# Optimization experiments

Hardware: AMD Instinct MI355X
Metric: run time of the kernel (lower is better)

The kernel has to match this reference:

```python
import jax, jax.numpy as jnp
import numpy as np

N = 100000
E = 1_600_000
DIN = 24
DH = 64
DOUT = 12
NEG_SLOPE = 0.01  # torch F.leaky_relu default


def setup_inputs() -> dict:
    key = jax.random.key(0)
    ks = jax.random.split(key, 18)
    inp = {}
    inp["feats"] = jax.random.normal(ks[0], (N, DIN), dtype=jnp.float32)
    inp["e_w"] = jax.random.uniform(ks[1], (E, 1), dtype=jnp.float32)
    inp["snorm_n"] = jnp.ones((N, 1), dtype=jnp.float32)
    inp["snorm_e"] = jnp.ones((E, 1), dtype=jnp.float32)
    inp["src"] = jax.random.randint(ks[2], (E,), 0, N, dtype=jnp.int32)
    inp["dst"] = jax.random.randint(ks[3], (E,), 0, N, dtype=jnp.int32)
    s = 0.05
    inp["emb_h_W"] = jax.random.normal(ks[4], (DH, DIN), dtype=jnp.float32) * s
    inp["emb_h_b"] = jnp.zeros((DH,), dtype=jnp.float32)
    inp["emb_e_W"] = jax.random.normal(ks[5], (DH, 1), dtype=jnp.float32) * s
    inp["emb_e_b"] = jnp.zeros((DH,), dtype=jnp.float32)
    inp["W_self1"] = jax.random.normal(ks[6], (DH, DH), dtype=jnp.float32) * s
    inp["W_func1"] = jax.random.normal(ks[7], (DH, DH), dtype=jnp.float32) * s
    inp["attn1"] = jax.random.normal(ks[8], (3 * DH,), dtype=jnp.float32) * s
    inp["W_self2"] = jax.random.normal(ks[9], (DH, DH), dtype=jnp.float32) * s
    inp["W_func2"] = jax.random.normal(ks[10], (DH, DH), dtype=jnp.float32) * s
    inp["attn2"] = jax.random.normal(ks[11], (3 * DH,), dtype=jnp.float32) * s
    inp["lin1_W"] = jax.random.normal(ks[12], (DOUT, DH), dtype=jnp.float32) * s
    inp["lin1_b"] = jnp.zeros((DOUT,), dtype=jnp.float32)
    return inp


def _gat_layer(h, w_edge, src, dst, W_self, W_func, attn):
    # h: [N, d], w_edge: [E, d] edge embedding, attn: [3d]
    h_s = h @ W_self.T                       # linear_self(h)
    z = h @ W_func.T                         # linear_func(h)
    d = z.shape[-1]
    a_src, a_dst, a_w = attn[:d], attn[d:2 * d], attn[2 * d:]
    # attention score: W_a . [z_src, z_dst, w]  (decomposed to avoid [E,3d] concat)
    s_node_src = z @ a_src                   # [N]
    s_node_dst = z @ a_dst                   # [N]
    e = s_node_src[src] + s_node_dst[dst] + w_edge @ a_w  # [E]
    e = jax.nn.leaky_relu(e, NEG_SLOPE)
    # segment softmax over incoming edges per destination node
    m = jax.ops.segment_max(e, dst, num_segments=h.shape[0])
    ex = jnp.exp(e - m[dst])
    denom = jax.ops.segment_sum(ex, dst, num_segments=h.shape[0])
    alpha = ex / denom[dst]                  # [E]
    msg = alpha[:, None] * z[src]            # [E, d]
    agg = jax.ops.segment_sum(msg, dst, num_segments=h.shape[0])  # [N, d]
    # DGL: nodes with no incoming edges keep their old 'h' (not h_s + agg)
    in_deg = jax.ops.segment_sum(jnp.ones_like(e), dst, num_segments=h.shape[0])
    h_mid = jnp.where((in_deg > 0)[:, None], h_s + agg, h)
    return h + jax.nn.relu(h_mid)            # relu then residual


def reference(feats, e_w, snorm_n, snorm_e, src, dst,
              emb_h_W, emb_h_b, emb_e_W, emb_e_b,
              W_self1, W_func1, attn1, W_self2, W_func2, attn2,
              lin1_W, lin1_b):
    feats = feats.reshape(feats.shape[0], -1)
    h = feats @ emb_h_W.T + emb_h_b          # [N, DH]
    e = e_w @ emb_e_W.T + emb_e_b            # [E, DH]
    h = _gat_layer(h, e, src, dst, W_self1, W_func1, attn1)
    h = _gat_layer(h, e, src, dst, W_self2, W_func2, attn2)
    y = h @ lin1_W.T + lin1_b                # [N, DOUT]
    return y
```

## Files before the change

### kernel.cpp

```cpp
#include <hip/hip_runtime.h>
#include <hip/hip_fp16.h>

#define N_NODES 100000
#define N_EDGES 1600000
#define DIN 24
#define DH 64
#define DOUT 12
#define NEG_SLOPE 0.01f
#define NG 32
#define EPG (N_EDGES / NG)
#define NS 7
#define SLICE_N 16384
#define NTOT (NG * N_NODES)
#define SCAN_BLK 4096
#define LDSW 72

#define NB_HIST (NS * NG)
#define NB_EMBED (((N_NODES * DH) + 8191) / 8192)
#define NB_SUMDEG ((N_NODES + 255) / 256)
#define NB_SCAN1N ((N_NODES + SCAN_BLK - 1) / SCAN_BLK)
#define NB_SCAT ((N_EDGES + 255) / 256)
#define NB_NODE ((N_NODES + 63) / 64)
#define NB_NODE_T ((NB_NODE + 1) / 2)
#define NB_AGG ((N_NODES + 7) / 8)

typedef _Float16 half8_t __attribute__((ext_vector_type(8)));
typedef float floatx4 __attribute__((ext_vector_type(4)));

__device__ __forceinline__ void dev_consts(const float* emb_e_W, const float* emb_e_b,
                                           const float* attn1, const float* attn2,
                                           float* consts) {
    int lane = threadIdx.x;
    if (lane >= 64) return;
    float w = emb_e_W[lane], b = emb_e_b[lane];
    float a1 = attn1[2 * DH + lane], a2 = attn2[2 * DH + lane];
    float c11 = w * a1, c01 = b * a1, c12 = w * a2, c02 = b * a2;
    for (int off = 32; off; off >>= 1) {
        c11 += __shfl_down(c11, off);
        c01 += __shfl_down(c01, off);
        c12 += __shfl_down(c12, off);
        c02 += __shfl_down(c02, off);
    }
    if (lane == 0) {
        consts[0] = c11; consts[1] = c01; consts[2] = c12; consts[3] = c02;
    }
}

__device__ __forceinline__ void dev_hist(int bid, const int* dst,
                                         unsigned char* deg, unsigned char* rank) {
    __shared__ unsigned cnt[SLICE_N / 4];
    int s = bid % NS, c = bid / NS;
    for (int i = threadIdx.x; i < SLICE_N / 4; i += 1024) cnt[i] = 0;
    __syncthreads();
    int nbase = s * SLICE_N;
    int start = c * EPG, end = start + EPG;
    for (int i = start + threadIdx.x; i < end; i += 1024) {
        int local = dst[i] - nbase;
        if ((unsigned)local < SLICE_N) {
            unsigned sh = (unsigned)(local & 3) * 8u;
            unsigned old = atomicAdd(&cnt[local >> 2], 1u << sh);
            rank[i] = (unsigned char)((old >> sh) & 255u);
        }
    }
    __syncthreads();
    int nmax = N_NODES - nbase;
    if (nmax > SLICE_N) nmax = SLICE_N;
    unsigned* dw = (unsigned*)(deg + (size_t)c * N_NODES + nbase);
    for (int l = threadIdx.x; l < (nmax >> 2); l += 1024) dw[l] = cnt[l];
}

__device__ __forceinline__ void dev_embed(int bid, const float* feats, const float* W,
                                          const float* b, float* h) {
    for (int r = 0; r < 8; ++r) {
        int idx = bid * 8192 + r * 1024 + threadIdx.x;
        if (idx >= N_NODES * DH) return;
        int n = idx >> 6, o = idx & 63;
        const float* f = feats + n * DIN;
        const float* w = W + o * DIN;
        float acc = b[o];
#pragma unroll
        for (int k = 0; k < DIN; ++k) acc += f[k] * w[k];
        h[idx] = acc;
    }
}

__device__ __forceinline__ void dev_scan1(int bid, const int* in, int* out,
                                          int* part, int n) {
    __shared__ int lds[256];
    int t = threadIdx.x;
    int base = bid * SCAN_BLK + t * 16;
    int v[16];
    int s = 0;
#pragma unroll
    for (int i = 0; i < 16; ++i) {
        int idx = base + i;
        v[i] = (idx < n) ? in[idx] : 0;
        s += v[i];
    }
    lds[t] = s;
    __syncthreads();
    for (int off = 1; off < 256; off <<= 1) {
        int y = (t >= off) ? lds[t - off] : 0;
        __syncthreads();
        lds[t] += y;
        __syncthreads();
    }
    int run = lds[t] - s;
#pragma unroll
    for (int i = 0; i < 16; ++i) {
        int idx = base + i;
        if (idx < n) out[idx] = run;
        run += v[i];
    }
    if (t == 255) part[bid] = lds[255];
}

__device__ __forceinline__ void dev_scan2(int* part, int nblk, int* row_offN) {
    __shared__ int lds2[256];
    int t = threadIdx.x;
    int v[4];
    int s = 0;
#pragma unroll
    for (int i = 0; i < 4; ++i) {
        int idx = t * 4 + i;
        v[i] = (idx < nblk) ? part[idx] : 0;
        s += v[i];
    }
    lds2[t] = s;
    __syncthreads();
    for (int off = 1; off < 256; off <<= 1) {
        int y = (t >= off) ? lds2[t - off] : 0;
        __syncthreads();
        lds2[t] += y;
        __syncthreads();
    }
    int run = lds2[t] - s;
#pragma unroll
    for (int i = 0; i < 4; ++i) {
        int idx = t * 4 + i;
        if (idx < nblk) part[idx] = run;
        run += v[i];
    }
    if (row_offN) {
        __syncthreads();
        if (t == 0) row_offN[N_NODES] = N_EDGES - part[N_NODES >> 12];
    }
}

__device__ __forceinline__ void dev_sumdeg(int bid, const unsigned char* degB,
                                           int* degN, unsigned char* chunkOff) {
    int n = bid * 256 + threadIdx.x;
    if (n >= N_NODES) return;
    int run = 0;
#pragma unroll
    for (int g = 0; g < NG; ++g) {
        size_t idx = (size_t)g * N_NODES + n;
        int v = (int)degB[idx];
        chunkOff[idx] = (unsigned char)run;
        run += v;
    }
    degN[n] = run;
}

__device__ __forceinline__ void dev_nodeM(int bid, int stride, const float* h,
                                          const float* Wself, const float* Wfunc,
                                          const float* attn,
                                          __half* zh, float* hs,
                                          float* s_src, float* s_dst) {
    __shared__ _Float16 lds[2 * 64 * LDSW];
    int tid = threadIdx.x;
    for (int idx = tid; idx < 2 * 64 * 64; idx += 256) {
        int mat = idx >> 12, rem = idx & 4095;
        int o = rem >> 6, k = rem & 63;
        float v = mat ? Wfunc[rem] : Wself[rem];
        lds[(mat * 64 + o) * LDSW + k] = (_Float16)v;
    }
    __syncthreads();

    int wave = tid >> 6, lane = tid & 63;
    int quad = lane >> 4, lm = lane & 15;
    float asv[4], adv[4];
#pragma unroll
    for (int t = 0; t < 4; ++t) {
        asv[t] = attn[t * 16 + lm];
        adv[t] = attn[DH + t * 16 + lm];
    }
    const _Float16* bS = lds;
    const _Float16* bF = lds + 64 * LDSW;

    for (int tb = bid; tb < NB_NODE; tb += stride) {
        int n0 = (tb * 4 + wave) * 16;
        if (n0 >= N_NODES) continue;

        half8_t afrag[2];
        {
            const float4* hrow = (const float4*)(h + (size_t)(n0 + lm) * DH);
#pragma unroll
            for (int ks = 0; ks < 2; ++ks) {
                float4 p0 = hrow[ks * 8 + quad * 2];
                float4 p1 = hrow[ks * 8 + quad * 2 + 1];
                half8_t a;
                a[0] = (_Float16)p0.x; a[1] = (_Float16)p0.y;
                a[2] = (_Float16)p0.z; a[3] = (_Float16)p0.w;
                a[4] = (_Float16)p1.x; a[5] = (_Float16)p1.y;
                a[6] = (_Float16)p1.z; a[7] = (_Float16)p1.w;
                afrag[ks] = a;
            }
        }

        floatx4 accS[4], accF[4];
#pragma unroll
        for (int t = 0; t < 4; ++t) { accS[t] = (floatx4)0.f; accF[t] = (floatx4)0.f; }

#pragma unroll
        for (int t = 0; t < 4; ++t) {
            int o = t * 16 + lm;
#pragma unroll
            for (int ks = 0; ks < 2; ++ks) {
                int hoff = o * LDSW + ks * 32 + quad * 8;
                half8_t b1 = *(const half8_t*)(bS + hoff);
                half8_t b2 = *(const half8_t*)(bF + hoff);
                accS[t] = __builtin_amdgcn_mfma_f32_16x16x32_f16(afrag[ks], b1, accS[t], 0, 0, 0);
                accF[t] = __builtin_amdgcn_mfma_f32_16x16x32_f16(afrag[ks], b2, accF[t], 0, 0, 0);
            }
        }

        float ps[4] = {0.f, 0.f, 0.f, 0.f}, pd[4] = {0.f, 0.f, 0.f, 0.f};
#pragma unroll
        for (int t = 0; t < 4; ++t) {
#pragma unroll
            for (int r = 0; r < 4; ++r) {
                int node = n0 + quad * 4 + r;
                float zv = accF[t][r];
                zh[(size_t)node * DH + t * 16 + lm] = __float2half(zv);
                hs[(size_t)node * DH + t * 16 + lm] = accS[t][r];
                ps[r] += zv * asv[t];
                pd[r] += zv * adv[t];
            }
        }
#pragma unroll
        for (int r = 0; r < 4; ++r) {
            float p1 = ps[r], p2 = pd[r];
            for (int off = 8; off; off >>= 1) {
                p1 += __shfl_xor(p1, off);
                p2 += __shfl_xor(p2, off);
            }
            if (lm == 0) {
                s_src[n0 + quad * 4 + r] = p1;
                s_dst[n0 + quad * 4 + r] = p2;
            }
        }
    }
}

__global__ void __launch_bounds__(1024, 2)
k_fuse1(const float* __restrict__ feats, const float* __restrict__ emb_h_W,
        const float* __restrict__ emb_h_b, float* __restrict__ h,
        const int* __restrict__ dst, unsigned char* __restrict__ deg,
        unsigned char* __restrict__ rank,
        const float* __restrict__ emb_e_W, const float* __restrict__ emb_e_b,
        const float* __restrict__ attn1, const float* __restrict__ attn2,
        float* __restrict__ consts) {
    int bid = blockIdx.x;
    if (bid == 0) { dev_consts(emb_e_W, emb_e_b, attn1, attn2, consts); return; }
    bid -= 1;
    if (bid < NB_HIST) { dev_hist(bid, dst, deg, rank); return; }
    dev_embed(bid - NB_HIST, feats, emb_h_W, emb_h_b, h);
}

__global__ void __launch_bounds__(256, 4)
k_fuse2(const unsigned char* __restrict__ degB, int* __restrict__ degN,
        unsigned char* __restrict__ chunkOff,
        const float* __restrict__ h, const float* __restrict__ Wself1,
        const float* __restrict__ Wfunc1, const float* __restrict__ attn1,
        __half* __restrict__ zh, float* __restrict__ hs,
        float* __restrict__ s_src, float* __restrict__ s_dst) {
    int bid = blockIdx.x;
    if (bid < NB_SUMDEG) { dev_sumdeg(bid, degB, degN, chunkOff); return; }
    dev_nodeM(bid - NB_SUMDEG, NB_NODE_T, h, Wself1, Wfunc1, attn1,
              zh, hs, s_src, s_dst);
}

__global__ void k_prep3(const int* __restrict__ degN, int* __restrict__ row_offN,
                        int* __restrict__ partN) {
    dev_scan1(blockIdx.x, degN, row_offN, partN, N_NODES);
}

__global__ void k_prep4(int* __restrict__ partN, int* __restrict__ row_offN) {
    dev_scan2(partN, NB_SCAN1N, row_offN);
}

__global__ void __launch_bounds__(256, 8)
k_scat(const int* __restrict__ src, const int* __restrict__ dst,
       const float* __restrict__ e_w, const unsigned char* __restrict__ rank,
       const int* __restrict__ row_offN, const int* __restrict__ partN,
       const unsigned char* __restrict__ chunkOff, unsigned* __restrict__ csr2) {
    int i = blockIdx.x * 256 + threadIdx.x;
    if (i >= N_EDGES) return;
    int g = i / EPG;
    int d = dst[i];
    unsigned qv = (unsigned)(e_w[i] * 32768.f);
    if (qv > 32767u) qv = 32767u;
    unsigned w = (unsigned)src[i] | (qv << 17);
    int pos = row_offN[d] + partN[d >> 12] + (int)chunkOff[(size_t)g * N_NODES + d]
            + (int)rank[i];
    csr2[pos] = w;
}

__global__ void __launch_bounds__(256, 4)
k_nodeL(const float* __restrict__ h, const float* __restrict__ Wself,
        const float* __restrict__ Wfunc, const float* __restrict__ attn,
        __half* __restrict__ zh, float* __restrict__ hs,
        float* __restrict__ s_src, float* __restrict__ s_dst) {
    dev_nodeM(blockIdx.x, NB_NODE_T, h, Wself, Wfunc, attn, zh, hs, s_src, s_dst);
}

__global__ void k_agg(const int* __restrict__ row_off, const int* __restrict__ partN,
                      const unsigned* __restrict__ csr,
                      const float* __restrict__ s_src, const float* __restrict__ s_dstA,
                      const float* __restrict__ consts, int layer,
                      const __half* __restrict__ zh, const float* __restrict__ hsb,
                      float* __restrict__ h,
                      const float* __restrict__ lin_W, const float* __restrict__ lin_b,
                      float* __restrict__ y, int final_layer) {
    int wave = threadIdx.x >> 6, lane = threadIdx.x & 63;
    int half = lane >> 5, hl = lane & 31;
    int eg = (lane >> 3) & 3, c8 = lane & 7;
    int n = blockIdx.x * 8 + wave * 2 + half;
    if (n >= N_NODES) return;
    int rs = row_off[n] + partN[n >> 12];
    int re = row_off[n + 1] + partN[(n + 1) >> 12];
    int deg = re - rs;
    int degO = __shfl_xor(deg, 32);
    int degmax = deg > degO ? deg : degO;

    float c1 = consts[layer * 2 + 0];
    float c0 = consts[layer * 2 + 1];
    float sd = s_dstA[n];

    float acc[8];
#pragma unroll
    for (int k = 0; k < 8; ++k) acc[k] = 0.f;
    float ssl = 0.f;
    int lbase = lane & 32;

    for (int base = 0; base < degmax; base += 32) {
        float ex = 0.f;
        int s0 = 0;
        int idx = base + hl;
        if (idx < deg) {
            unsigned w = csr[rs + idx];
            s0 = (int)(w & 0x1FFFFu);
            float ew = (float)(w >> 17) * (1.f / 32768.f);
            float e = s_src[s0] + sd + ew * c1 + c0;
            e = (e > 0.f) ? e : NEG_SLOPE * e;
            ex = __expf(e);
        }
        ssl += ex;
        int cnt = degmax - base;
        if (cnt > 32) cnt = 32;
#pragma unroll 4
        for (int jb = 0; jb < cnt; jb += 4) {
            int srcl = lbase + jb + eg;
            int sj = __shfl(s0, srcl);
            float exj = __shfl(ex, srcl);
            half8_t zv = *(const half8_t*)(zh + ((size_t)sj << 6) + (c8 << 3));
#pragma unroll
            for (int k = 0; k < 8; ++k) acc[k] += exj * (float)zv[k];
        }
    }
#pragma unroll
    for (int k = 0; k < 8; ++k) {
        acc[k] += __shfl_xor(acc[k], 8);
        acc[k] += __shfl_xor(acc[k], 16);
    }
    ssl += __shfl_xor(ssl, 16); ssl += __shfl_xor(ssl, 8);
    ssl += __shfl_xor(ssl, 4);  ssl += __shfl_xor(ssl, 2);
    ssl += __shfl_xor(ssl, 1);

    const float4* hp = (const float4*)(h + (size_t)n * DH);
    float4 ho0 = hp[c8 * 2], ho1 = hp[c8 * 2 + 1];
    float hold[8] = {ho0.x, ho0.y, ho0.z, ho0.w, ho1.x, ho1.y, ho1.z, ho1.w};
    float hnew[8];
    if (deg == 0) {
#pragma unroll
        for (int k = 0; k < 8; ++k) hnew[k] = hold[k] + fmaxf(hold[k], 0.f);
    } else {
        float rinv = 1.f / ssl;
        const float4* sp = (const float4*)(hsb + (size_t)n * DH);
        float4 hs0 = sp[c8 * 2], hs1 = sp[c8 * 2 + 1];
        float hsv[8] = {hs0.x, hs0.y, hs0.z, hs0.w, hs1.x, hs1.y, hs1.z, hs1.w};
#pragma unroll
        for (int k = 0; k < 8; ++k)
            hnew[k] = hold[k] + fmaxf(hsv[k] + acc[k] * rinv, 0.f);
    }

    if (!final_layer) {
        if (eg == 0) {
            float4* op = (float4*)(h + (size_t)n * DH);
            op[c8 * 2]     = make_float4(hnew[0], hnew[1], hnew[2], hnew[3]);
            op[c8 * 2 + 1] = make_float4(hnew[4], hnew[5], hnew[6], hnew[7]);
        }
    } else {
#pragma unroll
        for (int t = 0; t < 3; ++t) {
            int o = eg * 3 + t;
            const float* wr = lin_W + o * DH + c8 * 8;
            float p = 0.f;
#pragma unroll
            for (int k = 0; k < 8; ++k) p += hnew[k] * wr[k];
            p += __shfl_xor(p, 1); p += __shfl_xor(p, 2); p += __shfl_xor(p, 4);
            if (c8 == 0) y[n * DOUT + o] = p + lin_b[o];
        }
    }
}

extern "C" void kernel_launch(void* const* d_in, const int* in_sizes, int n_in,
                              void* d_out, int out_size, void* d_ws, size_t ws_size,
                              hipStream_t stream) {
    const float* feats   = (const float*)d_in[0];
    const float* e_w     = (const float*)d_in[1];
    const int*   src     = (const int*)d_in[4];
    const int*   dst     = (const int*)d_in[5];
    const float* emb_h_W = (const float*)d_in[6];
    const float* emb_h_b = (const float*)d_in[7];
    const float* emb_e_W = (const float*)d_in[8];
    const float* emb_e_b = (const float*)d_in[9];
    const float* Wself[2] = {(const float*)d_in[10], (const float*)d_in[13]};
    const float* Wfunc[2] = {(const float*)d_in[11], (const float*)d_in[14]};
    const float* attn[2]  = {(const float*)d_in[12], (const float*)d_in[15]};
    const float* lin1_W  = (const float*)d_in[16];
    const float* lin1_b  = (const float*)d_in[17];
    float* y = (float*)d_out;

    char* ws = (char*)d_ws;
    size_t off = 0;
    auto alloc = [&](size_t bytes) {
        void* p = ws + off;
        off += (bytes + 255) & ~(size_t)255;
        return p;
    };
    float*          h        = (float*)alloc((size_t)N_NODES * DH * 4);
    __half*         zh       = (__half*)alloc((size_t)N_NODES * DH * 2);
    float*          hs       = (float*)alloc((size_t)N_NODES * DH * 4);
    unsigned*       csr2     = (unsigned*)alloc((size_t)N_EDGES * 4);
    float*          s_src    = (float*)alloc((size_t)N_NODES * 4);
    float*          s_dst    = (float*)alloc((size_t)N_NODES * 4);
    int*            row_offN = (int*)alloc((size_t)(N_NODES + 1) * 4);
    unsigned char*  deg      = (unsigned char*)alloc((size_t)NTOT + 256);
    unsigned char*  chunkOff = (unsigned char*)alloc((size_t)NTOT + 256);
    unsigned char*  rank     = (unsigned char*)alloc((size_t)N_EDGES);
    int*            degN     = (int*)alloc((size_t)N_NODES * 4);
    int*            partN    = (int*)alloc(1024 * 4);
    float*          consts   = (float*)alloc(4 * 4);

    k_fuse1<<<1 + NB_HIST + NB_EMBED, 1024, 0, stream>>>(feats, emb_h_W, emb_h_b, h,
                                                         dst, deg, rank, emb_e_W, emb_e_b,
                                                         attn[0], attn[1], consts);
    k_fuse2<<<NB_SUMDEG + NB_NODE_T, 256, 0, stream>>>(
        deg, degN, chunkOff, h, Wself[0], Wfunc[0], attn[0], zh, hs, s_src, s_dst);
    k_prep3<<<NB_SCAN1N, 256, 0, stream>>>(degN, row_offN, partN);
    k_prep4<<<1, 256, 0, stream>>>(partN, row_offN);
    k_scat<<<NB_SCAT, 256, 0, stream>>>(src, dst, e_w, rank, row_offN, partN,
                                        chunkOff, csr2);
    k_agg<<<NB_AGG, 256, 0, stream>>>(row_offN, partN, csr2, s_src, s_dst, consts, 0,
                                      zh, hs, h, lin1_W, lin1_b, y, 0);
    k_nodeL<<<NB_NODE_T, 256, 0, stream>>>(h, Wself[1], Wfunc[1], attn[1],
                                           zh, hs, s_src, s_dst);
    k_agg<<<NB_AGG, 256, 0, stream>>>(row_offN, partN, csr2, s_src, s_dst, consts, 1,
                                      zh, hs, h, lin1_W, lin1_b, y, 1);
}
```

Measured before the change: 339.3 us.

## Fuse node embedding into first node-matmul kernel via MFMA and double histogram groups

```diff
diff --git a/kernel.cpp b/kernel.cpp
--- a/kernel.cpp
+++ b/kernel.cpp
@@ -7,7 +7,7 @@
 #define DH 64
 #define DOUT 12
 #define NEG_SLOPE 0.01f
-#define NG 32
+#define NG 64
 #define EPG (N_EDGES / NG)
 #define NS 7
 #define SLICE_N 16384
@@ -16,7 +16,6 @@
 #define LDSW 72
 
 #define NB_HIST (NS * NG)
-#define NB_EMBED (((N_NODES * DH) + 8191) / 8192)
 #define NB_SUMDEG ((N_NODES + 255) / 256)
 #define NB_SCAN1N ((N_NODES + SCAN_BLK - 1) / SCAN_BLK)
 #define NB_SCAT ((N_EDGES + 255) / 256)
@@ -69,21 +68,6 @@
     for (int l = threadIdx.x; l < (nmax >> 2); l += 1024) dw[l] = cnt[l];
 }
 
-__device__ __forceinline__ void dev_embed(int bid, const float* feats, const float* W,
-                                          const float* b, float* h) {
-    for (int r = 0; r < 8; ++r) {
-        int idx = bid * 8192 + r * 1024 + threadIdx.x;
-        if (idx >= N_NODES * DH) return;
-        int n = idx >> 6, o = idx & 63;
-        const float* f = feats + n * DIN;
-        const float* w = W + o * DIN;
-        float acc = b[o];
-#pragma unroll
-        for (int k = 0; k < DIN; ++k) acc += f[k] * w[k];
-        h[idx] = acc;
-    }
-}
-
 __device__ __forceinline__ void dev_scan1(int bid, const int* in, int* out,
                                           int* part, int n) {
     __shared__ int lds[256];
@@ -152,7 +136,6 @@
     int n = bid * 256 + threadIdx.x;
     if (n >= N_NODES) return;
     int run = 0;
-#pragma unroll
     for (int g = 0; g < NG; ++g) {
         size_t idx = (size_t)g * N_NODES + n;
         int v = (int)degB[idx];
@@ -160,6 +143,128 @@
         run += v;
     }
     degN[n] = run;
+}
+
+__device__ __forceinline__ void dev_nodeME(int bid, int stride,
+                                           const float* feats, const float* embW,
+                                           const float* embB,
+                                           const float* Wself, const float* Wfunc,
+                                           const float* attn,
+                                           float* h, __half* zh, float* hs,
+                                           float* s_src, float* s_dst) {
+    __shared__ _Float16 lds[2 * 64 * LDSW];
+    __shared__ _Float16 wembH[64 * 40];
+    __shared__ float biasS[64];
+    __shared__ _Float16 hbufH[4][16 * 72];
+    int tid = threadIdx.x;
+    for (int idx = tid; idx < 2 * 64 * 64; idx += 256) {
+        int mat = idx >> 12, rem = idx & 4095;
+        int o = rem >> 6, k = rem & 63;
+        float v = mat ? Wfunc[rem] : Wself[rem];
+        lds[(mat * 64 + o) * LDSW + k] = (_Float16)v;
+    }
+    for (int idx = tid; idx < 64 * 32; idx += 256) {
+        int o = idx >> 5, k = idx & 31;
+        wembH[o * 40 + k] = (_Float16)((k < DIN) ? embW[o * DIN + k] : 0.f);
+    }
+    if (tid < 64) biasS[tid] = embB[tid];
+    __syncthreads();
+
+    int wave = tid >> 6, lane = tid & 63;
+    int quad = lane >> 4, lm = lane & 15;
+    float asv[4], adv[4];
+#pragma unroll
+    for (int t = 0; t < 4; ++t) {
+        asv[t] = attn[t * 16 + lm];
+        adv[t] = attn[DH + t * 16 + lm];
+    }
+    const _Float16* bS = lds;
+    const _Float16* bF = lds + 64 * LDSW;
+    _Float16* hb = hbufH[wave];
+
+    for (int tb = bid; tb < NB_NODE; tb += stride) {
+        int n0 = (tb * 4 + wave) * 16;
+        if (n0 >= N_NODES) continue;
+
+        half8_t afE;
+#pragma unroll
+        for (int j = 0; j < 8; ++j) afE[j] = (_Float16)0.f;
+        if (quad < 3) {
+            const float* f = feats + (size_t)(n0 + lm) * DIN + quad * 8;
+            float4 q0 = *(const float4*)(f);
+            float4 q1 = *(const float4*)(f + 4);
+            afE[0] = (_Float16)q0.x; afE[1] = (_Float16)q0.y;
+            afE[2] = (_Float16)q0.z; afE[3] = (_Float16)q0.w;
+            afE[4] = (_Float16)q1.x; afE[5] = (_Float16)q1.y;
+            afE[6] = (_Float16)q1.z; afE[7] = (_Float16)q1.w;
+        }
+        floatx4 accE[4];
+#pragma unroll
+        for (int t = 0; t < 4; ++t) accE[t] = (floatx4)0.f;
+#pragma unroll
+        for (int t = 0; t < 4; ++t) {
+            int o = t * 16 + lm;
+            half8_t bE = *(const half8_t*)(wembH + o * 40 + quad * 8);
+            accE[t] = __builtin_amdgcn_mfma_f32_16x16x32_f16(afE, bE, accE[t], 0, 0, 0);
+        }
+#pragma unroll
+        for (int t = 0; t < 4; ++t) {
+            float bv = biasS[t * 16 + lm];
+#pragma unroll
+            for (int r = 0; r < 4; ++r) {
+                float hv = accE[t][r] + bv;
+                int node = n0 + quad * 4 + r;
+                h[(size_t)node * DH + t * 16 + lm] = hv;
+                hb[(quad * 4 + r) * 72 + t * 16 + lm] = (_Float16)hv;
+            }
+        }
+        half8_t afrag[2];
+#pragma unroll
+        for (int ks = 0; ks < 2; ++ks)
+            afrag[ks] = *(const half8_t*)(hb + lm * 72 + ks * 32 + quad * 8);
+
+        floatx4 accS[4], accF[4];
+#pragma unroll
+        for (int t = 0; t < 4; ++t) { accS[t] = (floatx4)0.f; accF[t] = (floatx4)0.f; }
+#pragma unroll
+        for (int t = 0; t < 4; ++t) {
+            int o = t * 16 + lm;
+#pragma unroll
+            for (int ks = 0; ks < 2; ++ks) {
+                int hoff = o * LDSW + ks * 32 + quad * 8;
+                half8_t b1 = *(const half8_t*)(bS + hoff);
+                half8_t b2 = *(const half8_t*)(bF + hoff);
+                accS[t] = __builtin_amdgcn_mfma_f32_16x16x32_f16(afrag[ks], b1, accS[t], 0, 0, 0);
+                accF[t] = __builtin_amdgcn_mfma_f32_16x16x32_f16(afrag[ks], b2, accF[t], 0, 0, 0);
+            }
+        }
+
+        float ps[4] = {0.f, 0.f, 0.f, 0.f}, pd[4] = {0.f, 0.f, 0.f, 0.f};
+#pragma unroll
+        for (int t = 0; t < 4; ++t) {
+#pragma unroll
+            for (int r = 0; r < 4; ++r) {
+                int node = n0 + quad * 4 + r;
+                float zv = accF[t][r];
+                zh[(size_t)node * DH + t * 16 + lm] = __float2half(zv);
+                hs[(size_t)node * DH + t * 16 + lm] = accS[t][r];
+                ps[r] += zv * asv[t];
+                pd[r] += zv * adv[t];
+            }
+        }
+#pragma unroll
+        for (int r = 0; r < 4; ++r) {
+            float p1 = ps[r], p2 = pd[r];
+            for (int off = 8; off; off >>= 1) {
+                p1 += __shfl_xor(p1, off);
+                p2 += __shfl_xor(p2, off);
+            }
+            if (lm == 0) {
+                s_src[n0 + quad * 4 + r] = p1;
+                s_dst[n0 + quad * 4 + r] = p2;
+            }
+        }
+    }
 }
 
 __device__ __forceinline__ void dev_nodeM(int bid, int stride, const float* h,
@@ -254,31 +359,32 @@
 }
 
 __global__ void __launch_bounds__(1024, 2)
-k_fuse1(const float* __restrict__ feats, const float* __restrict__ emb_h_W,
-        const float* __restrict__ emb_h_b, float* __restrict__ h,
-        const int* __restrict__ dst, unsigned char* __restrict__ deg,
+k_fuse1(const int* __restrict__ dst, unsigned char* __restrict__ deg,
         unsigned char* __restrict__ rank,
         const float* __restrict__ emb_e_W, const float* __restrict__ emb_e_b,
         const float* __restrict__ attn1, const float* __restrict__ attn2,
         float* __restrict__ consts) {
     int bid = blockIdx.x;
     if (bid == 0) { dev_consts(emb_e_W, emb_e_b, attn1, attn2, consts); return; }
-    bid -= 1;
-    if (bid < NB_HIST) { dev_hist(bid, dst, deg, rank); return; }
-    dev_embed(bid - NB_HIST, feats, emb_h_W, emb_h_b, h);
+    dev_hist(bid - 1, dst, deg, rank);
 }
 
 __global__ void __launch_bounds__(256, 4)
 k_fuse2(const unsigned char* __restrict__ degB, int* __restrict__ degN,
         unsigned char* __restrict__ chunkOff,
-        const float* __restrict__ h, const float* __restrict__ Wself1,
+        const float* __restrict__ feats, const float* __restrict__ embW,
+        const float* __restrict__ embB,
+        float* __restrict__ h, const float* __restrict__ Wself1,
         const float* __restrict__ Wfunc1, const float* __restrict__ attn1,
         __half* __restrict__ zh, float* __restrict__ hs,
         float* __restrict__ s_src, float* __restrict__ s_dst) {
     int bid = blockIdx.x;
-    if (bid < NB_SUMDEG) { dev_sumdeg(bid, degB, degN, chunkOff); return; }
-    dev_nodeM(bid - NB_SUMDEG, NB_NODE_T, h, Wself1, Wfunc1, attn1,
-              zh, hs, s_src, s_dst);
+    if (bid < NB_NODE_T) {
+        dev_nodeME(bid, NB_NODE_T, feats, embW, embB, Wself1, Wfunc1, attn1,
+                   h, zh, hs, s_src, s_dst);
+        return;
+    }
+    dev_sumdeg(bid - NB_NODE_T, degB, degN, chunkOff);
 }
 
 __global__ void k_prep3(const int* __restrict__ degN, int* __restrict__ row_offN,
@@ -454,11 +560,11 @@
     int*            partN    = (int*)alloc(1024 * 4);
     float*          consts   = (float*)alloc(4 * 4);
 
-    k_fuse1<<<1 + NB_HIST + NB_EMBED, 1024, 0, stream>>>(feats, emb_h_W, emb_h_b, h,
-                                                         dst, deg, rank, emb_e_W, emb_e_b,
-                                                         attn[0], attn[1], consts);
-    k_fuse2<<<NB_SUMDEG + NB_NODE_T, 256, 0, stream>>>(
-        deg, degN, chunkOff, h, Wself[0], Wfunc[0], attn[0], zh, hs, s_src, s_dst);
+    k_fuse1<<<1 + NB_HIST, 1024, 0, stream>>>(dst, deg, rank, emb_e_W, emb_e_b,
+                                              attn[0], attn[1], consts);
+    k_fuse2<<<NB_NODE_T + NB_SUMDEG, 256, 0, stream>>>(
+        deg, degN, chunkOff, feats, emb_h_W, emb_h_b,
+        h, Wself[0], Wfunc[0], attn[0], zh, hs, s_src, s_dst);
     k_prep3<<<NB_SCAN1N, 256, 0, stream>>>(degN, row_offN, partN);
     k_prep4<<<1, 256, 0, stream>>>(partN, row_offN);
     k_scat<<<NB_SCAT, 256, 0, stream>>>(src, dst, e_w, rank, row_offN, partN,
```

After: 305.6 us. -9.9%, faster.
